# Kernel optimization log

Measured on AMD Instinct MI355X. Metric: run time of the kernel, lower is better.

## Reference

```python
import jax, jax.numpy as jnp
import numpy as np


def setup_inputs() -> dict:
    key = jax.random.key(0)
    kq, kk, kv = jax.random.split(key, 3)
    B, Nq, Nk, d = 16, 4096, 4096, 128
    return {
        "query": jax.random.normal(kq, (B, Nq, d), dtype=jnp.float32),
        "key": jax.random.normal(kk, (B, Nk, d), dtype=jnp.float32),
        "value": jax.random.normal(kv, (B, Nk, d), dtype=jnp.float32),
    }


def reference(query, key, value):
    # weights = softmax(QK^T / sqrt(d)) with causal mask; dropout p=0.0 is identity
    d = key.shape[-1]
    scale = 1.0 / jnp.sqrt(jnp.asarray(d, dtype=query.dtype))
    scores = jnp.einsum("bqd,bkd->bqk", query, key) * scale  # [B, Nq, Nk]
    Nq, Nk = scores.shape[-2], scores.shape[-1]
    causal = jnp.tril(jnp.ones((Nq, Nk), dtype=bool))
    scores = jnp.where(causal, scores, jnp.asarray(-jnp.inf, dtype=scores.dtype))
    weights = jax.nn.softmax(scores, axis=-1)
    return jnp.einsum("bqk,bkv->bqv", weights, value)
```

## Files before the change

kernel.cpp:

```cpp
#include <hip/hip_runtime.h>
#include <stdint.h>


#define NB 16
#define NS 4096
#define DH 128
#define FRAG_U16 8192

typedef float          fx4   __attribute__((ext_vector_type(4)));
typedef uint32_t       ux4   __attribute__((ext_vector_type(4)));
typedef __bf16         bfv8  __attribute__((ext_vector_type(8)));
typedef __bf16         bfv4  __attribute__((ext_vector_type(4)));
typedef unsigned short u16x4 __attribute__((ext_vector_type(4)));

typedef const uint32_t __attribute__((address_space(1))) glob_u32;
typedef uint32_t       __attribute__((address_space(3))) lds_u32;

__device__ __forceinline__ fx4 mfma16(bfv8 a, bfv8 b, fx4 c) {
  return __builtin_amdgcn_mfma_f32_16x16x32_bf16(a, b, c, 0, 0, 0);
}

__global__ void __launch_bounds__(256) prepack_kernel(
    const float* __restrict__ K, const float* __restrict__ V,
    unsigned short* __restrict__ Kf, unsigned short* __restrict__ Vf) {
  __shared__ __align__(16) unsigned short tile[64][136];
  const int bid = blockIdx.x;
  const int b = bid >> 6, kvblk = bid & 63;
  const int kvb = kvblk << 6;
  const int tid = threadIdx.x;
  const size_t fbase = ((size_t)(b * 64 + kvblk)) * FRAG_U16;

  {
    const int tt = tid >> 6, lane = tid & 63;
    const int ln16 = lane & 15, g = lane >> 4;
    const float* kp = K + (((size_t)(b * NS + kvb + 16 * tt + ln16)) << 7) + 8 * g;
    unsigned short* op = Kf + fbase + tt * 2048 + lane * 8;
#pragma unroll
    for (int c = 0; c < 4; ++c) {
      fx4 a0 = *(const fx4*)(kp + 32 * c);
      fx4 a1 = *(const fx4*)(kp + 32 * c + 4);
      bfv8 t;
#pragma unroll
      for (int j = 0; j < 4; ++j) {
        t[j]     = (__bf16)a0[j];
        t[j + 4] = (__bf16)a1[j];
      }
      *(ux4*)(op + c * 512) = __builtin_bit_cast(ux4, t);
    }
  }

  {
    const int r = tid >> 2, cq = tid & 3;
    const float* vp = V + (((size_t)(b * NS + kvb + r)) << 7) + 32 * cq;
#pragma unroll
    for (int h = 0; h < 4; ++h) {
      fx4 f0 = *(const fx4*)(vp + 8 * h);
      fx4 f1 = *(const fx4*)(vp + 8 * h + 4);
      bfv8 t;
#pragma unroll
      for (int j = 0; j < 4; ++j) {
        t[j]     = (__bf16)f0[j];
        t[j + 4] = (__bf16)f1[j];
      }
      *(ux4*)&tile[r][32 * cq + 8 * h] = __builtin_bit_cast(ux4, t);
    }
  }
  __syncthreads();
  {
    const int dt = tid >> 5, c = (tid >> 4) & 1, ln16 = tid & 15;
    const int d = 16 * dt + ln16;
    unsigned short* op = Vf + fbase + dt * 1024 + c * 512 + ln16 * 8;
#pragma unroll
    for (int g = 0; g < 4; ++g) {
      unsigned short e[8];
#pragma unroll
      for (int j = 0; j < 4; ++j) {
        e[j]     = tile[32 * c + 4 * g + j][d];
        e[j + 4] = tile[32 * c + 16 + 4 * g + j][d];
      }
      *(ux4*)(op + g * 128) = *(const ux4*)e;
    }
  }
}

__global__ void __launch_bounds__(256, 3) attn_kernel(
    const float* __restrict__ Q, const unsigned short* __restrict__ Kf,
    const unsigned short* __restrict__ Vf, float* __restrict__ O,
    unsigned short* __restrict__ Pa, float* __restrict__ Ml, int split) {
  __shared__ __align__(16) unsigned char sm[32768];

  const int wid  = blockIdx.x;
  const int tid  = threadIdx.x;
  const int w    = tid >> 6;
  const int lane = tid & 63;
  const int g    = lane >> 4;
  const int ln16 = lane & 15;

  int b;
  int t, u0, un, mode, pidx, slot;
  int t1 = 0, u1a = 0, u1b = 0, m1v = 0;
  int again = 0;

  if (split) {
    const int n = wid >> 4;
    b = wid & 15;
    const int v = n / 3;
    const int k = n - 3 * v;
    const int L = 128 - 4 * v;
    const int st = 44 * k, en = st + 44;
    if (st < L) {
      t = 31 - v; u0 = st; un = (en < L) ? en : L;
      mode = (k == 0) ? 1 : 2;
      slot = k;
      pidx = (t <= 21) ? (t - 11) : (11 + 2 * (t - 22) + (k - 1));
      if (en > L) {
        t1 = v; u1a = 0; u1b = en - L;
        m1v = (v <= 10) ? 0 : 1;
        again = 1;
      }
    } else {
      t = v; u0 = st - L; un = en - L;
      const int s = (u0 > 0) ? 1 : 0;
      mode = (v <= 10) ? 0 : ((s == 0) ? 1 : 2);
      slot = s;
      pidx = v - 11;
    }
  } else {
    const int half = wid >> 8, ii = wid & 255;
    b = ii & 15;
    const int qi = ii >> 4;
    t = half ? qi : 31 - qi;
    u0 = 0; un = 4 * t + 4; mode = 0; pidx = 0; slot = 0;
  }

  const float SCALE = 0.12753102f;
  const fx4 z4 = {0.f, 0.f, 0.f, 0.f};

  const unsigned char* kfB = (const unsigned char*)Kf + (size_t)b * 1048576;
  const unsigned char* vfB = (const unsigned char*)Vf + (size_t)b * 1048576;

#define STAGE(jb, bo)                                                          \
  do {                                                                         \
    const unsigned char* gk = kfB + (size_t)(jb) * 8192;                       \
    const unsigned char* gv = vfB + (size_t)((jb) >> 1) * 16384 + ((jb) & 1) * 1024; \
    _Pragma("unroll")                                                          \
    for (int ii = 0; ii < 2; ++ii) {                                           \
      __builtin_amdgcn_global_load_lds(                                        \
          (glob_u32*)(gk + w * 2048 + ii * 1024 + lane * 16),                  \
          (lds_u32*)(sm + (bo) + w * 2048 + ii * 1024), 16, 0, 0);             \
      const int dt_ = 2 * w + ii;                                              \
      __builtin_amdgcn_global_load_lds(                                        \
          (glob_u32*)(gv + dt_ * 2048 + lane * 16),                            \
          (lds_u32*)(sm + (bo) + 8192 + dt_ * 1024), 16, 0, 0);                \
    }                                                                          \
  } while (0)

  for (;;) {
    const int qw = (t << 7) + 32 * w;

    bfv8 qf[2][4];
#pragma unroll
    for (int qt = 0; qt < 2; ++qt) {
#pragma unroll
      for (int c = 0; c < 4; ++c) {
        const float* qp = Q + (((size_t)(b * NS + qw + qt * 16 + ln16)) << 7) + 32 * c + 8 * g;
        fx4 a0 = *(const fx4*)qp;
        fx4 a1 = *(const fx4*)(qp + 4);
        bfv8 tt_;
#pragma unroll
        for (int j = 0; j < 4; ++j) {
          tt_[j]     = (__bf16)(a0[j] * SCALE);
          tt_[j + 4] = (__bf16)(a1[j] * SCALE);
        }
        qf[qt][c] = tt_;
      }
    }

    fx4 acc[2][8];
#pragma unroll
    for (int qt = 0; qt < 2; ++qt)
#pragma unroll
      for (int dt = 0; dt < 8; ++dt) acc[qt][dt] = z4;
    float mrun[2] = {-1e30f, -1e30f};
    float lsum[2] = {0.f, 0.f};

    const int nkvw = (qw >> 5) + 1;

    STAGE(u0, 0);
    asm volatile("s_waitcnt vmcnt(0)" ::: "memory");
    __builtin_amdgcn_s_barrier();
    asm volatile("" ::: "memory");

    int cur = 0;
    for (int jb = u0; jb < un; ++jb) {
      if (jb + 1 < un) STAGE(jb + 1, (cur ^ 1) * 16384);

      if (jb < nkvw) {
        const unsigned char* kb = sm + cur * 16384;
        const unsigned char* vb = kb + 8192;

        fx4 s[2][2];
        s[0][0] = z4; s[0][1] = z4; s[1][0] = z4; s[1][1] = z4;
        __builtin_amdgcn_s_setprio(1);
#pragma unroll
        for (int tt = 0; tt < 2; ++tt) {
#pragma unroll
          for (int c = 0; c < 4; ++c) {
            bfv8 kfr = *(const bfv8*)(kb + tt * 4096 + c * 1024 + lane * 16);
            s[0][tt] = mfma16(kfr, qf[0][c], s[0][tt]);
            s[1][tt] = mfma16(kfr, qf[1][c], s[1][tt]);
          }
        }
        __builtin_amdgcn_s_setprio(0);

        const int kvb = jb << 5;
        if (kvb + 31 > qw) {
#pragma unroll
          for (int qt = 0; qt < 2; ++qt) {
            const int qrow = qw + qt * 16 + ln16;
#pragma unroll
            for (int tt = 0; tt < 2; ++tt)
#pragma unroll
              for (int r = 0; r < 4; ++r) {
                int kvpos = kvb + 16 * tt + 4 * g + r;
                if (kvpos > qrow) s[qt][tt][r] = -1e30f;
              }
          }
        }

        bfv8 pb[2];
#pragma unroll
        for (int qt = 0; qt < 2; ++qt) {
          fx4 m4 = __builtin_elementwise_max(s[qt][0], s[qt][1]);
          float pm = fmaxf(fmaxf(m4[0], m4[1]), fmaxf(m4[2], m4[3]));
          pm = fmaxf(pm, __shfl_xor(pm, 16));
          pm = fmaxf(pm, __shfl_xor(pm, 32));
          float mq = mrun[qt];
          if (__any(pm > mq + 8.0f)) {
            float mn = fmaxf(mq, pm);
            float f  = __builtin_amdgcn_exp2f(mq - mn);
            lsum[qt] *= f;
#pragma unroll
            for (int dt = 0; dt < 8; ++dt) acc[qt][dt] *= f;
            mrun[qt] = mn;
            mq = mn;
          }
#pragma unroll
          for (int tt = 0; tt < 2; ++tt)
#pragma unroll
            for (int r = 0; r < 4; ++r)
              s[qt][tt][r] = __builtin_amdgcn_exp2f(s[qt][tt][r] - mq);
          fx4 r4 = s[qt][0] + s[qt][1];
          float rs = (r4[0] + r4[1]) + (r4[2] + r4[3]);
          rs += __shfl_xor(rs, 16);
          rs += __shfl_xor(rs, 32);
          lsum[qt] += rs;
          bfv8 tt_;
#pragma unroll
          for (int j = 0; j < 4; ++j) {
            tt_[j]     = (__bf16)s[qt][0][j];
            tt_[j + 4] = (__bf16)s[qt][1][j];
          }
          pb[qt] = tt_;
        }

        __builtin_amdgcn_s_setprio(1);
#pragma unroll
        for (int dt = 0; dt < 8; ++dt) {
          bfv8 vfr = *(const bfv8*)(vb + dt * 1024 + lane * 16);
          acc[0][dt] = mfma16(vfr, pb[0], acc[0][dt]);
          acc[1][dt] = mfma16(vfr, pb[1], acc[1][dt]);
        }
        __builtin_amdgcn_s_setprio(0);
      }

      asm volatile("s_waitcnt vmcnt(0)" ::: "memory");
      __builtin_amdgcn_s_barrier();
      asm volatile("" ::: "memory");
      cur ^= 1;
    }

    if (mode == 0) {
#pragma unroll
      for (int qt = 0; qt < 2; ++qt) {
        float inv = 1.0f / lsum[qt];
        float* ob = O + (((size_t)(b * NS + qw + qt * 16 + ln16)) << 7) + 4 * g;
#pragma unroll
        for (int dt = 0; dt < 8; ++dt) *(fx4*)(ob + 16 * dt) = acc[qt][dt] * inv;
      }
    } else {
      if (mode == 1) {
#pragma unroll
        for (int qt = 0; qt < 2; ++qt) {
          float* ob = O + (((size_t)(b * NS + qw + qt * 16 + ln16)) << 7) + 4 * g;
#pragma unroll
          for (int dt = 0; dt < 8; ++dt) *(fx4*)(ob + 16 * dt) = acc[qt][dt];
        }
      } else {
#pragma unroll
        for (int qt = 0; qt < 2; ++qt) {
          const int row = 32 * w + 16 * qt + ln16;
          unsigned short* pp =
              Pa + (((size_t)((b * 32 + pidx) * 128 + row)) << 7) + 4 * g;
#pragma unroll
          for (int dt = 0; dt < 8; ++dt) {
            bfv4 t4;
#pragma unroll
            for (int j = 0; j < 4; ++j) t4[j] = (__bf16)acc[qt][dt][j];
            *(u16x4*)(pp + 16 * dt) = __builtin_bit_cast(u16x4, t4);
          }
        }
      }
      if (g == 0) {
        float* mlp = Ml + (size_t)((b * 32 + t) * 4 + slot) * 256;
#pragma unroll
        for (int qt = 0; qt < 2; ++qt) {
          const int row = 32 * w + 16 * qt + ln16;
          mlp[row]       = mrun[qt];
          mlp[128 + row] = lsum[qt];
        }
      }
    }

    if (!again) break;
    again = 0;
    t = t1; u0 = u1a; un = u1b; mode = m1v; pidx = 0; slot = 0;
  }
#undef STAGE
}

__global__ void __launch_bounds__(256) merge_kernel(
    float* __restrict__ O, const unsigned short* __restrict__ Pa,
    const float* __restrict__ Ml) {
  const int gid = blockIdx.x * 256 + threadIdx.x;
  const int d4  = gid & 31;
  const int rg  = gid >> 5;
  const int b   = rg / 2688;
  const int r2  = rg - b * 2688;
  const int ti  = r2 >> 7;
  const int row = r2 & 127;
  const int t   = 11 + ti;

  const float* mlb = Ml + (size_t)((b * 32 + t) * 4) * 256;
  const float m0 = mlb[row],       l0 = mlb[128 + row];
  const float m1 = mlb[256 + row], l1 = mlb[384 + row];
  const int three = (t >= 22);
  float m2 = -1e30f, l2 = 0.f;
  if (three) { m2 = mlb[512 + row]; l2 = mlb[640 + row]; }

  const float m  = fmaxf(fmaxf(m0, m1), m2);
  const float w0 = __builtin_amdgcn_exp2f(m0 - m);
  const float w1 = __builtin_amdgcn_exp2f(m1 - m);

  float* op = O + (((size_t)(b * NS + (t << 7) + row)) << 7) + 4 * d4;
  fx4 a0 = *(const fx4*)op;

  const int p1 = (t <= 21) ? (t - 11) : (11 + 2 * (t - 22));
  const unsigned short* pp1 =
      Pa + (((size_t)((b * 32 + p1) * 128 + row)) << 7) + 4 * d4;
  bfv4 a1b = __builtin_bit_cast(bfv4, *(const u16x4*)pp1);
  fx4 a1;
#pragma unroll
  for (int j = 0; j < 4; ++j) a1[j] = (float)a1b[j];

  fx4 num   = a0 * w0 + a1 * w1;
  float den = w0 * l0 + w1 * l1;
  if (three) {
    const float w2 = __builtin_amdgcn_exp2f(m2 - m);
    const unsigned short* pp2 =
        Pa + (((size_t)((b * 32 + p1 + 1) * 128 + row)) << 7) + 4 * d4;
    bfv4 a2b = __builtin_bit_cast(bfv4, *(const u16x4*)pp2);
    fx4 a2;
#pragma unroll
    for (int j = 0; j < 4; ++j) a2[j] = (float)a2b[j];
    num += a2 * w2;
    den += w2 * l2;
  }
  *(fx4*)op = num * (1.0f / den);
}

extern "C" void kernel_launch(void* const* d_in, const int* in_sizes, int n_in,
                              void* d_out, int out_size, void* d_ws, size_t ws_size,
                              hipStream_t stream) {
  (void)in_sizes; (void)n_in; (void)out_size;
  const float* Q = (const float*)d_in[0];
  const float* K = (const float*)d_in[1];
  const float* V = (const float*)d_in[2];
  float* O = (float*)d_out;

  unsigned short* Kf = (unsigned short*)d_ws;
  unsigned short* Vf = Kf + (size_t)NB * NS * DH;
  unsigned short* Pa = (unsigned short*)((char*)d_ws + 33554432);
  float*          Ml = (float*)((char*)d_ws + 50331648);

  const size_t NEED = 52428800;
  const int split = (ws_size >= NEED) ? 1 : 0;

  prepack_kernel<<<dim3(NB * 64), dim3(256), 0, stream>>>(K, V, Kf, Vf);
  attn_kernel<<<dim3(split ? 768 : 512), dim3(256), 0, stream>>>(
      Q, Kf, Vf, O, Pa, Ml, split);
  if (split) merge_kernel<<<dim3(5376), dim3(256), 0, stream>>>(O, Pa, Ml);
}
```

Measured before the change: 125.1 us.

## Replace LDS double-buffered K/V staging with direct per-wave global fragment loads

Drops the shared-memory double buffer filled with global_load_lds and the per-iteration barriers. Each wave now reads K and V fragments straight from global memory (through L2/L1). The V prepack layout is changed so a 32-key block is contiguous, and V fragments are loaded before the masking and softmax work so their latency is hidden. This also lets each wave stop at its own causal limit instead of stepping through the block-wide range. The cost is that the four waves no longer share K/V through LDS, so every wave re-reads the same fragments from cache. Memory-level latency hiding now depends on occupancy and the early V loads rather than on explicit prefetching.

```diff
diff --git a/kernel.cpp b/kernel.cpp
--- a/kernel.cpp
+++ b/kernel.cpp
@@ -5,16 +5,12 @@
 #define NB 16
 #define NS 4096
 #define DH 128
-#define FRAG_U16 8192
 
 typedef float          fx4   __attribute__((ext_vector_type(4)));
 typedef uint32_t       ux4   __attribute__((ext_vector_type(4)));
 typedef __bf16         bfv8  __attribute__((ext_vector_type(8)));
 typedef __bf16         bfv4  __attribute__((ext_vector_type(4)));
 typedef unsigned short u16x4 __attribute__((ext_vector_type(4)));
-
-typedef const uint32_t __attribute__((address_space(1))) glob_u32;
-typedef uint32_t       __attribute__((address_space(3))) lds_u32;
 
 __device__ __forceinline__ fx4 mfma16(bfv8 a, bfv8 b, fx4 c) {
   return __builtin_amdgcn_mfma_f32_16x16x32_bf16(a, b, c, 0, 0, 0);
@@ -28,7 +24,7 @@
   const int b = bid >> 6, kvblk = bid & 63;
   const int kvb = kvblk << 6;
   const int tid = threadIdx.x;
-  const size_t fbase = ((size_t)(b * 64 + kvblk)) * FRAG_U16;
+  const size_t fbase = ((size_t)(b * 64 + kvblk)) * 8192;
 
   {
     const int tt = tid >> 6, lane = tid & 63;
@@ -69,7 +65,7 @@
   {
     const int dt = tid >> 5, c = (tid >> 4) & 1, ln16 = tid & 15;
     const int d = 16 * dt + ln16;
-    unsigned short* op = Vf + fbase + dt * 1024 + c * 512 + ln16 * 8;
+    unsigned short* op = Vf + fbase + c * 4096 + dt * 512 + ln16 * 8;
 #pragma unroll
     for (int g = 0; g < 4; ++g) {
       unsigned short e[8];
@@ -87,8 +83,6 @@
     const float* __restrict__ Q, const unsigned short* __restrict__ Kf,
     const unsigned short* __restrict__ Vf, float* __restrict__ O,
     unsigned short* __restrict__ Pa, float* __restrict__ Ml, int split) {
-  __shared__ __align__(16) unsigned char sm[32768];
-
   const int wid  = blockIdx.x;
   const int tid  = threadIdx.x;
   const int w    = tid >> 6;
@@ -139,22 +133,6 @@
   const unsigned char* kfB = (const unsigned char*)Kf + (size_t)b * 1048576;
   const unsigned char* vfB = (const unsigned char*)Vf + (size_t)b * 1048576;
 
-#define STAGE(jb, bo)                                                          \
-  do {                                                                         \
-    const unsigned char* gk = kfB + (size_t)(jb) * 8192;                       \
-    const unsigned char* gv = vfB + (size_t)((jb) >> 1) * 16384 + ((jb) & 1) * 1024; \
-    _Pragma("unroll")                                                          \
-    for (int ii = 0; ii < 2; ++ii) {                                           \
-      __builtin_amdgcn_global_load_lds(                                        \
-          (glob_u32*)(gk + w * 2048 + ii * 1024 + lane * 16),                  \
-          (lds_u32*)(sm + (bo) + w * 2048 + ii * 1024), 16, 0, 0);             \
-      const int dt_ = 2 * w + ii;                                              \
-      __builtin_amdgcn_global_load_lds(                                        \
-          (glob_u32*)(gv + dt_ * 2048 + lane * 16),                            \
-          (lds_u32*)(sm + (bo) + 8192 + dt_ * 1024), 16, 0, 0);                \
-    }                                                                          \
-  } while (0)
-
   for (;;) {
     const int qw = (t << 7) + 32 * w;
 
@@ -185,99 +163,87 @@
     float lsum[2] = {0.f, 0.f};
 
     const int nkvw = (qw >> 5) + 1;
-
-    STAGE(u0, 0);
-    asm volatile("s_waitcnt vmcnt(0)" ::: "memory");
-    __builtin_amdgcn_s_barrier();
-    asm volatile("" ::: "memory");
-
-    int cur = 0;
-    for (int jb = u0; jb < un; ++jb) {
-      if (jb + 1 < un) STAGE(jb + 1, (cur ^ 1) * 16384);
-
-      if (jb < nkvw) {
-        const unsigned char* kb = sm + cur * 16384;
-        const unsigned char* vb = kb + 8192;
-
-        fx4 s[2][2];
-        s[0][0] = z4; s[0][1] = z4; s[1][0] = z4; s[1][1] = z4;
-        __builtin_amdgcn_s_setprio(1);
-#pragma unroll
-        for (int tt = 0; tt < 2; ++tt) {
-#pragma unroll
-          for (int c = 0; c < 4; ++c) {
-            bfv8 kfr = *(const bfv8*)(kb + tt * 4096 + c * 1024 + lane * 16);
-            s[0][tt] = mfma16(kfr, qf[0][c], s[0][tt]);
-            s[1][tt] = mfma16(kfr, qf[1][c], s[1][tt]);
-          }
-        }
-        __builtin_amdgcn_s_setprio(0);
-
-        const int kvb = jb << 5;
-        if (kvb + 31 > qw) {
-#pragma unroll
-          for (int qt = 0; qt < 2; ++qt) {
-            const int qrow = qw + qt * 16 + ln16;
-#pragma unroll
-            for (int tt = 0; tt < 2; ++tt)
-#pragma unroll
-              for (int r = 0; r < 4; ++r) {
-                int kvpos = kvb + 16 * tt + 4 * g + r;
-                if (kvpos > qrow) s[qt][tt][r] = -1e30f;
-              }
-          }
-        }
-
-        bfv8 pb[2];
+    const int jend = (un < nkvw) ? un : nkvw;
+
+    for (int jb = u0; jb < jend; ++jb) {
+      const unsigned char* ku = kfB + (size_t)jb * 8192;
+      const unsigned char* vu = vfB + (size_t)jb * 8192;
+
+      fx4 s[2][2];
+      s[0][0] = z4; s[0][1] = z4; s[1][0] = z4; s[1][1] = z4;
+      __builtin_amdgcn_s_setprio(1);
+#pragma unroll
+      for (int tt = 0; tt < 2; ++tt) {
+#pragma unroll
+        for (int c = 0; c < 4; ++c) {
+          bfv8 kfr = *(const bfv8*)(ku + tt * 4096 + c * 1024 + lane * 16);
+          s[0][tt] = mfma16(kfr, qf[0][c], s[0][tt]);
+          s[1][tt] = mfma16(kfr, qf[1][c], s[1][tt]);
+        }
+      }
+      __builtin_amdgcn_s_setprio(0);
+
+      bfv8 vfr[8];
+#pragma unroll
+      for (int dt = 0; dt < 8; ++dt)
+        vfr[dt] = *(const bfv8*)(vu + dt * 1024 + lane * 16);
+
+      const int kvb = jb << 5;
+      if (kvb + 31 > qw) {
 #pragma unroll
         for (int qt = 0; qt < 2; ++qt) {
-          fx4 m4 = __builtin_elementwise_max(s[qt][0], s[qt][1]);
-          float pm = fmaxf(fmaxf(m4[0], m4[1]), fmaxf(m4[2], m4[3]));
-          pm = fmaxf(pm, __shfl_xor(pm, 16));
-          pm = fmaxf(pm, __shfl_xor(pm, 32));
-          float mq = mrun[qt];
-          if (__any(pm > mq + 8.0f)) {
-            float mn = fmaxf(mq, pm);
-            float f  = __builtin_amdgcn_exp2f(mq - mn);
-            lsum[qt] *= f;
-#pragma unroll
-            for (int dt = 0; dt < 8; ++dt) acc[qt][dt] *= f;
-            mrun[qt] = mn;
-            mq = mn;
-          }
+          const int qrow = qw + qt * 16 + ln16;
 #pragma unroll
           for (int tt = 0; tt < 2; ++tt)
 #pragma unroll
-            for (int r = 0; r < 4; ++r)
-              s[qt][tt][r] = __builtin_amdgcn_exp2f(s[qt][tt][r] - mq);
-          fx4 r4 = s[qt][0] + s[qt][1];
-          float rs = (r4[0] + r4[1]) + (r4[2] + r4[3]);
-          rs += __shfl_xor(rs, 16);
-          rs += __shfl_xor(rs, 32);
-          lsum[qt] += rs;
-          bfv8 tt_;
-#pragma unroll
-          for (int j = 0; j < 4; ++j) {
-            tt_[j]     = (__bf16)s[qt][0][j];
-            tt_[j + 4] = (__bf16)s[qt][1][j];
-          }
-          pb[qt] = tt_;
-        }
-
-        __builtin_amdgcn_s_setprio(1);
-#pragma unroll
-        for (int dt = 0; dt < 8; ++dt) {
-          bfv8 vfr = *(const bfv8*)(vb + dt * 1024 + lane * 16);
-          acc[0][dt] = mfma16(vfr, pb[0], acc[0][dt]);
-          acc[1][dt] = mfma16(vfr, pb[1], acc[1][dt]);
-        }
-        __builtin_amdgcn_s_setprio(0);
-      }
-
-      asm volatile("s_waitcnt vmcnt(0)" ::: "memory");
-      __builtin_amdgcn_s_barrier();
-      asm volatile("" ::: "memory");
-      cur ^= 1;
+            for (int r = 0; r < 4; ++r) {
+              int kvpos = kvb + 16 * tt + 4 * g + r;
+              if (kvpos > qrow) s[qt][tt][r] = -1e30f;
+            }
+        }
+      }
+
+      bfv8 pb[2];
+#pragma unroll
+      for (int qt = 0; qt < 2; ++qt) {
+        fx4 m4 = __builtin_elementwise_max(s[qt][0], s[qt][1]);
+        float pm = fmaxf(fmaxf(m4[0], m4[1]), fmaxf(m4[2], m4[3]));
+        pm = fmaxf(pm, __shfl_xor(pm, 16));
+        pm = fmaxf(pm, __shfl_xor(pm, 32));
+        if (__any(pm > mrun[qt] + 8.0f)) {
+          float mn = fmaxf(mrun[qt], pm);
+          float f  = __builtin_amdgcn_exp2f(mrun[qt] - mn);
+          lsum[qt] *= f;
+#pragma unroll
+          for (int dt = 0; dt < 8; ++dt) acc[qt][dt] *= f;
+          mrun[qt] = mn;
+        }
+#pragma unroll
+        for (int tt = 0; tt < 2; ++tt)
+#pragma unroll
+          for (int r = 0; r < 4; ++r)
+            s[qt][tt][r] = __builtin_amdgcn_exp2f(s[qt][tt][r] - mrun[qt]);
+        fx4 r4 = s[qt][0] + s[qt][1];
+        float rs = (r4[0] + r4[1]) + (r4[2] + r4[3]);
+        rs += __shfl_xor(rs, 16);
+        rs += __shfl_xor(rs, 32);
+        lsum[qt] += rs;
+        bfv8 tt_;
+#pragma unroll
+        for (int j = 0; j < 4; ++j) {
+          tt_[j]     = (__bf16)s[qt][0][j];
+          tt_[j + 4] = (__bf16)s[qt][1][j];
+        }
+        pb[qt] = tt_;
+      }
+
+      __builtin_amdgcn_s_setprio(1);
+#pragma unroll
+      for (int dt = 0; dt < 8; ++dt) {
+        acc[0][dt] = mfma16(vfr[dt], pb[0], acc[0][dt]);
+        acc[1][dt] = mfma16(vfr[dt], pb[1], acc[1][dt]);
+      }
+      __builtin_amdgcn_s_setprio(0);
     }
 
     if (mode == 0) {
@@ -326,7 +292,6 @@
     again = 0;
     t = t1; u0 = u1a; un = u1b; mode = m1v; pidx = 0; slot = 0;
   }
-#undef STAGE
 }
 
 __global__ void __launch_bounds__(256) merge_kernel(
```

After: 133.1 us. 6.4% more time.
